# Kernel tuning notes

Hardware: AMD Instinct MI355X
Metric: run time of the kernel (lower is better)

Reference implementation:

```python
import jax, jax.numpy as jnp
import numpy as np

N = 50000
E = 400000
F_IN = 128
HID = 64
HEADS = 4
OUT_HEADS = 4
N_CLS = 121
NEG_SLOPE = 0.2


def _gat_layer(x, src, dst, W, a_src, a_dst, b, heads, out_ch, concat):
    n = x.shape[0]
    xh = (x @ W).reshape(n, heads, out_ch)                      # [N,H,C]
    alpha_s = jnp.sum(xh * a_src, axis=-1)                      # [N,H]
    alpha_d = jnp.sum(xh * a_dst, axis=-1)                      # [N,H]
    logits = jax.nn.leaky_relu(alpha_s[src] + alpha_d[dst], NEG_SLOPE)  # [E,H]
    # numerically stable edge softmax per destination node
    m = jax.ops.segment_max(logits, dst, num_segments=n)        # [N,H]
    e = jnp.exp(logits - m[dst])                                # [E,H]
    denom = jax.ops.segment_sum(e, dst, num_segments=n)         # [N,H]
    alpha = e / (denom[dst] + 1e-16)                            # [E,H]
    msg = alpha[:, :, None] * xh[src]                           # [E,H,C]
    out = jax.ops.segment_sum(msg, dst, num_segments=n)         # [N,H,C]
    if concat:
        out = out.reshape(n, heads * out_ch)
    else:
        out = out.mean(axis=1)
    return out + b


def setup_inputs() -> dict:
    key = jax.random.key(0)
    ks = jax.random.split(key, 20)
    x = jax.random.normal(ks[0], (N, F_IN), dtype=jnp.float32)
    edge_index = jax.random.randint(ks[1], (2, E), 0, N, dtype=jnp.int32)
    s = lambda *sh: 1.0 / np.sqrt(sh[0])
    inp = {
        'x': x,
        'edge_index': edge_index,
        # conv1: F_IN -> HEADS*HID
        'W1': jax.random.normal(ks[2], (F_IN, HEADS * HID), jnp.float32) * s(F_IN),
        'a1_src': jax.random.normal(ks[3], (HEADS, HID), jnp.float32) * s(HID),
        'a1_dst': jax.random.normal(ks[4], (HEADS, HID), jnp.float32) * s(HID),
        'b1': jnp.zeros((HEADS * HID,), jnp.float32),
        'lin1_W': jax.random.normal(ks[5], (F_IN, HEADS * HID), jnp.float32) * s(F_IN),
        'lin1_b': jnp.zeros((HEADS * HID,), jnp.float32),
        # conv2: HEADS*HID -> HEADS*HID
        'W2': jax.random.normal(ks[6], (HEADS * HID, HEADS * HID), jnp.float32) * s(HEADS * HID),
        'a2_src': jax.random.normal(ks[7], (HEADS, HID), jnp.float32) * s(HID),
        'a2_dst': jax.random.normal(ks[8], (HEADS, HID), jnp.float32) * s(HID),
        'b2': jnp.zeros((HEADS * HID,), jnp.float32),
        # conv3: HEADS*HID -> N_CLS (mean over OUT_HEADS)
        'W3': jax.random.normal(ks[9], (HEADS * HID, OUT_HEADS * N_CLS), jnp.float32) * s(HEADS * HID),
        'a3_src': jax.random.normal(ks[10], (OUT_HEADS, N_CLS), jnp.float32) * s(N_CLS),
        'a3_dst': jax.random.normal(ks[11], (OUT_HEADS, N_CLS), jnp.float32) * s(N_CLS),
        'b3': jnp.zeros((N_CLS,), jnp.float32),
        'lin3_W': jax.random.normal(ks[12], (HEADS * HID, N_CLS), jnp.float32) * s(HEADS * HID),
        'lin3_b': jnp.zeros((N_CLS,), jnp.float32),
    }
    return inp


def reference(x, edge_index, W1, a1_src, a1_dst, b1, lin1_W, lin1_b,
              W2, a2_src, a2_dst, b2, W3, a3_src, a3_dst, b3, lin3_W, lin3_b):
    src, dst = edge_index[0], edge_index[1]
    h = _gat_layer(x, src, dst, W1, a1_src, a1_dst, b1, HEADS, HID, True) + (x @ lin1_W + lin1_b)
    h = jax.nn.elu(h)
    h = _gat_layer(h, src, dst, W2, a2_src, a2_dst, b2, HEADS, HID, True) + h  # residual skip (no lin2)
    h = jax.nn.elu(h)
    out = _gat_layer(h, src, dst, W3, a3_src, a3_dst, b3, OUT_HEADS, N_CLS, False) + (h @ lin3_W + lin3_b)
    return out
```

## Files before the change

kernel.cpp:

```cpp
#include <hip/hip_runtime.h>
#include <cstdint>
#include <cstddef>

#define F_IN 128
#define HC12 256
#define HC3P 512
#define NCLS 121
#define L3STR 128

typedef unsigned short u16;
typedef unsigned int u32;
typedef __attribute__((ext_vector_type(8))) short short8;
typedef __attribute__((ext_vector_type(8))) __fp16 half8;
typedef __attribute__((ext_vector_type(4))) float float4v;

static __device__ __forceinline__ float lrelu(float x) { return x > 0.f ? x : 0.2f * x; }

static __device__ __forceinline__ u16 f2h(float f) {
    union { __fp16 h; u16 u; } v; v.h = (__fp16)f; return v.u;
}
static __device__ __forceinline__ float h2f(u16 u) {
    union { u16 u; __fp16 h; } v; v.u = u; return (float)v.h;
}

static __device__ __forceinline__ void gload16(const u16* g, u16* l) {
    __builtin_amdgcn_global_load_lds((const __attribute__((address_space(1))) void*)g,
                                     (__attribute__((address_space(3))) void*)l,
                                     16, 0, 0);
}

__global__ void hist_kernel(const int* __restrict__ dst, int* __restrict__ deg, int E) {
    int e = blockIdx.x * 256 + threadIdx.x;
    if (e < E) atomicAdd(&deg[dst[e]], 1);
}

__global__ __launch_bounds__(1024) void scan_kernel(const int* __restrict__ deg,
                                                    int* __restrict__ rowp, int N) {
    __shared__ int swave[16];
    __shared__ int s_carry;
    int tid = threadIdx.x;
    int w = tid >> 6, lane = tid & 63;
    if (tid == 0) { rowp[0] = 0; s_carry = 0; }
    __syncthreads();
    for (int base = 0; base < N; base += 4096) {
        int i0 = base + tid * 4;
        int v0 = (i0     < N) ? deg[i0]     : 0;
        int v1 = (i0 + 1 < N) ? deg[i0 + 1] : 0;
        int v2 = (i0 + 2 < N) ? deg[i0 + 2] : 0;
        int v3 = (i0 + 3 < N) ? deg[i0 + 3] : 0;
        int t = v0 + v1 + v2 + v3;
        int sc = t;
#pragma unroll
        for (int off = 1; off < 64; off <<= 1) {
            int u = __shfl_up(sc, off, 64);
            if (lane >= off) sc += u;
        }
        if (lane == 63) swave[w] = sc;
        __syncthreads();
        if (w == 0) {
            int ws = (lane < 16) ? swave[lane] : 0;
#pragma unroll
            for (int off = 1; off < 16; off <<= 1) {
                int u = __shfl_up(ws, off, 64);
                if (lane >= off) ws += u;
            }
            if (lane < 16) swave[lane] = ws;
        }
        __syncthreads();
        int carry = s_carry;
        int tb = carry + ((w > 0) ? swave[w - 1] : 0) + sc - t;
        if (i0     < N) rowp[i0 + 1] = tb + v0;
        if (i0 + 1 < N) rowp[i0 + 2] = tb + v0 + v1;
        if (i0 + 2 < N) rowp[i0 + 3] = tb + v0 + v1 + v2;
        if (i0 + 3 < N) rowp[i0 + 4] = tb + t;
        __syncthreads();
        if (tid == 1023) s_carry = carry + swave[15];
        __syncthreads();
    }
}

__global__ void scatter_kernel(const int* __restrict__ src, const int* __restrict__ dst,
                               const int* __restrict__ rowp, int* __restrict__ cur,
                               int* __restrict__ col, int E) {
    int e = blockIdx.x * 256 + threadIdx.x;
    if (e < E) {
        int d = dst[e];
        int pos = rowp[d] + atomicAdd(&cur[d], 1);
        col[pos] = src[e];
    }
}

__global__ void cvtT_all_kernel(const float* W1, const float* l1W, const float* W2,
                                const float* W3, const float* l3W,
                                const float* a3s, const float* a3d,
                                u16* C1, u16* C2, u16* C3,
                                float* as3p, float* ad3p) {
    int i = blockIdx.x * 256 + threadIdx.x;
    if (i >= 285952) {
        int j = i - 285952;
        if (j < 1024) {
            int t = j >> 9, k = j & 511;
            int h = k >> 7, c = k & 127;
            const float* a = t ? a3d : a3s;
            float v = (c < NCLS) ? a[h * NCLS + c] : 0.f;
            (t ? ad3p : as3p)[k] = v;
        }
        return;
    }
    const float* B; u16* o; int K, N;
    if (i < 32768)       { B = W1;  o = C1;             K = 128; N = 256; }
    else if (i < 65536)  { B = l1W; o = C1 + 256 * 128; K = 128; N = 256; i -= 32768; }
    else if (i < 131072) { B = W2;  o = C2;             K = 256; N = 256; i -= 65536; }
    else if (i < 254976) { B = W3;  o = C3;             K = 256; N = 484; i -= 131072; }
    else                 { B = l3W; o = C3 + 484 * 256; K = 256; N = 121; i -= 254976; }
    int n = i % N, k = i / N;
    o[(size_t)n * K + k] = f2h(B[(size_t)k * N + n]);
}

__global__ __launch_bounds__(256) void xcvt_kernel(const float* __restrict__ x,
                                                   u16* __restrict__ o, int total8) {
    int i = blockIdx.x * 256 + threadIdx.x;
    if (i >= total8) return;
    const float4* p = (const float4*)(x + (size_t)i * 8);
    float4 a = p[0], b = p[1];
    union { u16 u[8]; short8 v; } r;
    r.u[0] = f2h(a.x); r.u[1] = f2h(a.y); r.u[2] = f2h(a.z); r.u[3] = f2h(a.w);
    r.u[4] = f2h(b.x); r.u[5] = f2h(b.y); r.u[6] = f2h(b.z); r.u[7] = f2h(b.w);
    *(short8*)(o + (size_t)i * 8) = r.v;
}

#define BM 128
#define BN 128
#define BK 32

__global__ __launch_bounds__(256, 3) void gemm_f16(const u16* __restrict__ A16,
                                                   const u16* __restrict__ BT,
                                                   int M, int K, int Ntot,
                                                   int nx, int ny,
                                                   int Nb, u16* __restrict__ Cb, int strideB,
                                                   int pad121,
                                                   u16* __restrict__ Cf16,
                                                   const float* __restrict__ biasf, int strideF) {
    __shared__ __align__(16) u16 sA[BM * BK];
    __shared__ __align__(16) u16 sB[BN * BK];
    int tid = threadIdx.x;
    int wave = tid >> 6, lane = tid & 63;
    int wr = wave >> 1, wc = wave & 1;

    int bid = blockIdx.x;
    int G = nx * 8;
    int g = bid / G;
    int rem = ny - g * 8;
    int rb, cb;
    if (rem >= 8) {
        int r = bid - g * G;
        rb = g * 8 + (r & 7);
        cb = r >> 3;
    } else {
        int t = bid - g * G;
        rb = g * 8 + t % rem;
        cb = t / rem;
    }
    int m0 = rb * BM, n0 = cb * BN;

    int fm = lane & 15;
    int q = lane >> 4;

    int srow = lane >> 2;
    int sch = (lane & 3) * 8;
    u16* lA0 = &sA[(wave * 32) * BK];
    u16* lA1 = &sA[(wave * 32 + 16) * BK];
    u16* lB0 = &sB[(wave * 32) * BK];
    u16* lB1 = &sB[(wave * 32 + 16) * BK];
    int ar0 = min(m0 + wave * 32 + srow, M - 1);
    int ar1 = min(m0 + wave * 32 + 16 + srow, M - 1);
    int br0 = min(n0 + wave * 32 + srow, Ntot - 1);
    int br1 = min(n0 + wave * 32 + 16 + srow, Ntot - 1);

    float4v acc[4][4];
#pragma unroll
    for (int i = 0; i < 4; i++)
#pragma unroll
        for (int j = 0; j < 4; j++) acc[i][j] = (float4v){0.f, 0.f, 0.f, 0.f};

    for (int kc = 0; kc < K; kc += BK) {
        gload16(&A16[(size_t)ar0 * K + kc + sch], lA0);
        gload16(&A16[(size_t)ar1 * K + kc + sch], lA1);
        gload16(&BT[(size_t)br0 * K + kc + sch], lB0);
        gload16(&BT[(size_t)br1 * K + kc + sch], lB1);
        __syncthreads();

        half8 ah[4];
#pragma unroll
        for (int mi = 0; mi < 4; mi++)
            ah[mi] = *(const half8*)&sA[(wr * 64 + mi * 16 + fm) * BK + q * 8];
#pragma unroll
        for (int ni = 0; ni < 4; ni++) {
            half8 bh = *(const half8*)&sB[(wc * 64 + ni * 16 + fm) * BK + q * 8];
#pragma unroll
            for (int mi = 0; mi < 4; mi++)
                acc[mi][ni] = __builtin_amdgcn_mfma_f32_16x16x32_f16(ah[mi], bh, acc[mi][ni], 0, 0, 0);
        }
        __syncthreads();
    }

#pragma unroll
    for (int mi = 0; mi < 4; mi++) {
#pragma unroll
        for (int ni = 0; ni < 4; ni++) {
            int colg = n0 + wc * 64 + ni * 16 + fm;
            if (colg >= Ntot) continue;
            int cg = colg;
            if (pad121 && colg < Nb) {
                int hh = (colg * 1084) >> 17;
                cg = colg + 7 * hh;
            }
#pragma unroll
            for (int r = 0; r < 4; r++) {
                int rowg = m0 + wr * 64 + mi * 16 + q * 4 + r;
                if (rowg >= M) continue;
                float v = acc[mi][ni][r];
                if (colg < Nb) {
                    Cb[(size_t)rowg * strideB + cg] = f2h(v);
                } else {
                    int cf = colg - Nb;
                    Cf16[(size_t)rowg * strideF + cf] = f2h(v + biasf[cf]);
                }
            }
        }
    }
}

__global__ __launch_bounds__(256) void alpha_wave_256(const u16* __restrict__ xh,
                                                      const float* __restrict__ a_s,
                                                      const float* __restrict__ a_d,
                                                      float* __restrict__ as_o,
                                                      float* __restrict__ ad_o, int N) {
    int lane = threadIdx.x & 63;
    int n = blockIdx.x * 4 + (threadIdx.x >> 6);
    if (n >= N) return;
    int c = lane * 4;
    uint2 v = *(const uint2*)&xh[(size_t)n * HC12 + c];
    float4 s4 = *(const float4*)&a_s[c];
    float4 d4 = *(const float4*)&a_d[c];
    float x0 = h2f((u16)(v.x & 0xffff)), x1 = h2f((u16)(v.x >> 16));
    float x2 = h2f((u16)(v.y & 0xffff)), x3 = h2f((u16)(v.y >> 16));
    float ss = x0 * s4.x + x1 * s4.y + x2 * s4.z + x3 * s4.w;
    float sd = x0 * d4.x + x1 * d4.y + x2 * d4.z + x3 * d4.w;
#pragma unroll
    for (int o = 1; o < 16; o <<= 1) {
        ss += __shfl_xor(ss, o, 64);
        sd += __shfl_xor(sd, o, 64);
    }
    if ((lane & 15) == 0) {
        as_o[n * 4 + (lane >> 4)] = ss;
        ad_o[n * 4 + (lane >> 4)] = sd;
    }
}

__global__ __launch_bounds__(256) void alpha3_wave(const u16* __restrict__ xh3,
                                                   const float* __restrict__ as3p,
                                                   const float* __restrict__ ad3p,
                                                   float* __restrict__ as_o,
                                                   float* __restrict__ ad_o, int N) {
    int l = threadIdx.x & 63;
    int n = blockIdx.x * 4 + (threadIdx.x >> 6);
    if (n >= N) return;
    int h = l >> 4, li = l & 15;
    int c0 = li * 8;
    uint4 v = *(const uint4*)&xh3[(size_t)n * HC3P + l * 8];
    float4 s0 = *(const float4*)&as3p[l * 8];
    float4 s1 = *(const float4*)&as3p[l * 8 + 4];
    float4 d0 = *(const float4*)&ad3p[l * 8];
    float4 d1 = *(const float4*)&ad3p[l * 8 + 4];
    u32 ww[4] = {v.x, v.y, v.z, v.w};
    float xs[8];
#pragma unroll
    for (int j = 0; j < 8; j++) {
        float xf = h2f((u16)((ww[j >> 1] >> ((j & 1) * 16)) & 0xffff));
        xs[j] = (c0 + j < NCLS) ? xf : 0.f;
    }
    float ss = xs[0] * s0.x + xs[1] * s0.y + xs[2] * s0.z + xs[3] * s0.w
             + xs[4] * s1.x + xs[5] * s1.y + xs[6] * s1.z + xs[7] * s1.w;
    float sd = xs[0] * d0.x + xs[1] * d0.y + xs[2] * d0.z + xs[3] * d0.w
             + xs[4] * d1.x + xs[5] * d1.y + xs[6] * d1.z + xs[7] * d1.w;
#pragma unroll
    for (int o = 1; o < 16; o <<= 1) {
        ss += __shfl_xor(ss, o, 64);
        sd += __shfl_xor(sd, o, 64);
    }
    if (li == 0) {
        as_o[n * 4 + h] = ss;
        ad_o[n * 4 + h] = sd;
    }
}

__global__ __launch_bounds__(256) void stats_wave(const int* __restrict__ rowp,
                                                  const int* __restrict__ col,
                                                  const float* __restrict__ asrc,
                                                  const float* __restrict__ adst,
                                                  float* __restrict__ alphaE, int N) {
    int l = threadIdx.x & 63;
    int n = blockIdx.x * 4 + (threadIdx.x >> 6);
    if (n >= N) return;
    int r0 = rowp[n], r1 = rowp[n + 1];
    if (r0 == r1) return;
    int h = l & 3, el = l >> 2;
    float ad = adst[n * 4 + h];
    if (r1 - r0 <= 16) {
        int e = r0 + el;
        bool v = e < r1;
        int sc = col[v ? e : r0];
        float lg = lrelu(asrc[sc * 4 + h] + ad);
        float m = v ? lg : -3.4e38f;
#pragma unroll
        for (int o = 4; o < 64; o <<= 1) m = fmaxf(m, __shfl_xor(m, o, 64));
        float ex = v ? __expf(lg - m) : 0.f;
        float s = ex;
#pragma unroll
        for (int o = 4; o < 64; o <<= 1) s += __shfl_xor(s, o, 64);
        if (v) alphaE[(size_t)e * 4 + h] = ex / (s + 1e-16f);
    } else {
        float m = -3.4e38f, s = 0.f;
        for (int kb = r0; kb < r1; kb += 16) {
            int e = kb + el;
            bool v = e < r1;
            int sc = col[v ? e : r0];
            float lg = lrelu(asrc[sc * 4 + h] + ad);
            float cm = v ? lg : -3.4e38f;
#pragma unroll
            for (int o = 4; o < 64; o <<= 1) cm = fmaxf(cm, __shfl_xor(cm, o, 64));
            float nm = fmaxf(m, cm);
            float ex = v ? __expf(lg - nm) : 0.f;
            float cs = ex;
#pragma unroll
            for (int o = 4; o < 64; o <<= 1) cs += __shfl_xor(cs, o, 64);
            s = s * __expf(m - nm) + cs;
            m = nm;
        }
        float rd = 1.f / (s + 1e-16f);
        for (int kb = r0; kb < r1; kb += 16) {
            int e = kb + el;
            if (e < r1) {
                int sc = col[e];
                float lg = lrelu(asrc[sc * 4 + h] + ad);
                alphaE[(size_t)e * 4 + h] = __expf(lg - m) * rd;
            }
        }
    }
}

__global__ __launch_bounds__(256) void agg_wave_256(const u16* __restrict__ xh,
                                                    const int* __restrict__ rowp,
                                                    const int* __restrict__ col,
                                                    const float* __restrict__ alphaE,
                                                    const float* __restrict__ bias,
                                                    const u16* __restrict__ res16,
                                                    u16* __restrict__ out16, int N) {
    int l = threadIdx.x & 63;
    int n = blockIdx.x * 4 + (threadIdx.x >> 6);
    if (n >= N) return;
    int r0 = rowp[n], r1 = rowp[n + 1];
    int s = l >> 5, li = l & 31;
    int c = li * 8;
    int h = li >> 3;
    float acc[8] = {0.f, 0.f, 0.f, 0.f, 0.f, 0.f, 0.f, 0.f};
    for (int kb = r0; kb < r1; kb += 16) {
        int cn = min(16, r1 - kb);
        int cidx = col[kb + (l & 15)];
        float alv = alphaE[(size_t)kb * 4 + l];
        int npair = (cn + 1) >> 1;
#pragma unroll 4
        for (int k = 0; k < npair; k++) {
            int e = 2 * k + s;
            int em = e < cn ? e : cn - 1;
            int src = __shfl(cidx, em, 64);
            float al = __shfl(alv, em * 4 + h, 64);
            if (e >= cn) al = 0.f;
            uint4 v = *(const uint4*)&xh[(size_t)src * HC12 + c];
            acc[0] += al * h2f((u16)(v.x & 0xffff));
            acc[1] += al * h2f((u16)(v.x >> 16));
            acc[2] += al * h2f((u16)(v.y & 0xffff));
            acc[3] += al * h2f((u16)(v.y >> 16));
            acc[4] += al * h2f((u16)(v.z & 0xffff));
            acc[5] += al * h2f((u16)(v.z >> 16));
            acc[6] += al * h2f((u16)(v.w & 0xffff));
            acc[7] += al * h2f((u16)(v.w >> 16));
        }
    }
#pragma unroll
    for (int j = 0; j < 8; j++) acc[j] += __shfl_xor(acc[j], 32, 64);
    if (l < 32) {
        uint4 rv = *(const uint4*)&res16[(size_t)n * HC12 + c];
        u32 rw[4] = {rv.x, rv.y, rv.z, rv.w};
        float4 b0 = *(const float4*)&bias[c];
        float4 b1v = *(const float4*)&bias[c + 4];
        float bb[8] = {b0.x, b0.y, b0.z, b0.w, b1v.x, b1v.y, b1v.z, b1v.w};
        union { u16 u[8]; uint4 v; } p;
#pragma unroll
        for (int j = 0; j < 8; j++) {
            float rf = h2f((u16)((rw[j >> 1] >> ((j & 1) * 16)) & 0xffff));
            float vv = acc[j] + bb[j] + rf;
            float ev = vv > 0.f ? vv : expm1f(vv);
            p.u[j] = f2h(ev);
        }
        *(uint4*)&out16[(size_t)n * HC12 + c] = p.v;
    }
}

__global__ __launch_bounds__(256) void agg_wave_out(const u16* __restrict__ xh3,
                                                    const int* __restrict__ rowp,
                                                    const int* __restrict__ col,
                                                    const float* __restrict__ alphaE,
                                                    const float* __restrict__ b3,
                                                    const u16* __restrict__ lin3h,
                                                    float* __restrict__ out, int N) {
    int l = threadIdx.x & 63;
    int half = l >> 5, li = l & 31;
    int bl = l & 32;
    int n = blockIdx.x * 8 + (threadIdx.x >> 6) * 2 + half;
    bool nv = n < N;
    int r0 = nv ? rowp[n] : 0;
    int r1 = nv ? rowp[n + 1] : 0;
    float acc[16];
#pragma unroll
    for (int j = 0; j < 16; j++) acc[j] = 0.f;
    for (int kb = r0; kb < r1; kb += 8) {
        int ec = min(8, r1 - kb);
        int ce = kb + (li & 7);
        int cidx = col[ce < r1 ? ce : r0];
        float alv = alphaE[(size_t)kb * 4 + li];
        for (int k = 0; k < ec; k++) {
            int src = __shfl(cidx, bl + k, 64);
            float al = __shfl(alv, bl + k * 4 + (li >> 3), 64);
            const u16* row = xh3 + (size_t)src * HC3P + li * 16;
            uint4 v0 = *(const uint4*)&row[0];
            uint4 v1 = *(const uint4*)&row[8];
            u32 w0[4] = {v0.x, v0.y, v0.z, v0.w};
            u32 w1[4] = {v1.x, v1.y, v1.z, v1.w};
#pragma unroll
            for (int jj = 0; jj < 4; jj++) {
                acc[2 * jj]     += al * h2f((u16)(w0[jj] & 0xffff));
                acc[2 * jj + 1] += al * h2f((u16)(w0[jj] >> 16));
                acc[8 + 2 * jj]     += al * h2f((u16)(w1[jj] & 0xffff));
                acc[8 + 2 * jj + 1] += al * h2f((u16)(w1[jj] >> 16));
            }
        }
    }
#pragma unroll
    for (int j = 0; j < 16; j++) {
        acc[j] += __shfl_xor(acc[j], 8, 64);
        acc[j] += __shfl_xor(acc[j], 16, 64);
    }
    if (nv && li < 8) {
        int c0 = li * 16;
        uint4 l0 = *(const uint4*)&lin3h[(size_t)n * L3STR + c0];
        uint4 l1 = *(const uint4*)&lin3h[(size_t)n * L3STR + c0 + 8];
        u32 lw[8] = {l0.x, l0.y, l0.z, l0.w, l1.x, l1.y, l1.z, l1.w};
#pragma unroll
        for (int j = 0; j < 16; j++) {
            int cc = c0 + j;
            if (cc < NCLS) {
                float lf = h2f((u16)((lw[j >> 1] >> ((j & 1) * 16)) & 0xffff));
                out[(size_t)n * NCLS + cc] = 0.25f * acc[j] + b3[cc] + lf;
            }
        }
    }
}

extern "C" void kernel_launch(void* const* d_in, const int* in_sizes, int n_in,
                              void* d_out, int out_size, void* d_ws, size_t ws_size,
                              hipStream_t stream) {
    const float* x   = (const float*)d_in[0];
    const int*   ei  = (const int*)d_in[1];
    const float* W1  = (const float*)d_in[2];
    const float* a1s = (const float*)d_in[3];
    const float* a1d = (const float*)d_in[4];
    const float* b1  = (const float*)d_in[5];
    const float* l1W = (const float*)d_in[6];
    const float* l1b = (const float*)d_in[7];
    const float* W2  = (const float*)d_in[8];
    const float* a2s = (const float*)d_in[9];
    const float* a2d = (const float*)d_in[10];
    const float* b2  = (const float*)d_in[11];
    const float* W3  = (const float*)d_in[12];
    const float* a3s = (const float*)d_in[13];
    const float* a3d = (const float*)d_in[14];
    const float* b3  = (const float*)d_in[15];
    const float* l3W = (const float*)d_in[16];
    const float* l3b = (const float*)d_in[17];

    const int N = in_sizes[0] / F_IN;
    const int E = in_sizes[1] / 2;
    const int* srcv = ei;
    const int* dstv = ei + E;

    char* ws = (char*)d_ws;
    size_t off = 0;
    auto alloc = [&](size_t bytes) -> char* {
        char* p = ws + off;
        off += (bytes + 255) & ~(size_t)255;
        return p;
    };
    u16*   xh    = (u16*)alloc((size_t)N * HC3P * 2 + 256);
    u16*   x16   = (u16*)alloc((size_t)N * F_IN * 2);
    u16*   h1f   = (u16*)alloc((size_t)N * HC12 * 2);
    u16*   h2f   = (u16*)alloc((size_t)N * HC12 * 2);
    u16*   lin1h = (u16*)alloc((size_t)N * HC12 * 2);
    u16*   lin3h = (u16*)alloc((size_t)N * L3STR * 2);
    float* as_   = (float*)alloc((size_t)N * 4 * 4);
    float* ad_   = (float*)alloc((size_t)N * 4 * 4);
    int* rowp    = (int*)alloc((size_t)(N + 1) * 4);
    int* degc    = (int*)alloc((size_t)N * 4);
    int* cur     = (int*)alloc((size_t)N * 4);
    int* col     = (int*)alloc((size_t)E * 4 + 256);
    float* alphaE = (float*)alloc((size_t)E * 4 * 4 + 256);
    u16* C1 = (u16*)alloc((size_t)512 * 128 * 2);
    u16* C2 = (u16*)alloc((size_t)256 * 256 * 2);
    u16* C3 = (u16*)alloc((size_t)605 * 256 * 2);
    float* as3p = (float*)alloc(512 * 4);
    float* ad3p = (float*)alloc(512 * 4);
    (void)ws_size; (void)n_in; (void)out_size;

    hipMemsetAsync(degc, 0, (size_t)N * 4, stream);
    hipMemsetAsync(cur, 0, (size_t)N * 4, stream);
    hist_kernel<<<(E + 255) / 256, 256, 0, stream>>>(dstv, degc, E);
    scan_kernel<<<1, 1024, 0, stream>>>(degc, rowp, N);
    scatter_kernel<<<(E + 255) / 256, 256, 0, stream>>>(srcv, dstv, rowp, cur, col, E);

    cvtT_all_kernel<<<(285952 + 1024 + 255) / 256, 256, 0, stream>>>(W1, l1W, W2, W3, l3W,
                                                                     a3s, a3d, C1, C2, C3,
                                                                     as3p, ad3p);
    xcvt_kernel<<<(N * F_IN / 8 + 255) / 256, 256, 0, stream>>>(x, x16, N * F_IN / 8);

    int ny = (N + BM - 1) / BM;
    int wgrid = (N + 3) / 4;
    int wgrid8 = (N + 7) / 8;

    gemm_f16<<<4 * ny, 256, 0, stream>>>(x16, C1, N, F_IN, 512, 4, ny,
                                         256, xh, 256, 0, lin1h, l1b, 256);
    alpha_wave_256<<<wgrid, 256, 0, stream>>>(xh, a1s, a1d, as_, ad_, N);
    stats_wave<<<wgrid, 256, 0, stream>>>(rowp, col, as_, ad_, alphaE, N);
    agg_wave_256<<<wgrid, 256, 0, stream>>>(xh, rowp, col, alphaE, b1, lin1h, h1f, N);

    gemm_f16<<<2 * ny, 256, 0, stream>>>(h1f, C2, N, HC12, 256, 2, ny,
                                         256, xh, 256, 0, nullptr, nullptr, 0);
    alpha_wave_256<<<wgrid, 256, 0, stream>>>(xh, a2s, a2d, as_, ad_, N);
    stats_wave<<<wgrid, 256, 0, stream>>>(rowp, col, as_, ad_, alphaE, N);
    agg_wave_256<<<wgrid, 256, 0, stream>>>(xh, rowp, col, alphaE, b2, h1f, h2f, N);

    gemm_f16<<<5 * ny, 256, 0, stream>>>(h2f, C3, N, HC12, 605, 5, ny,
                                         484, xh, HC3P, 1, lin3h, l3b, L3STR);
    alpha3_wave<<<wgrid, 256, 0, stream>>>(xh, as3p, ad3p, as_, ad_, N);
    stats_wave<<<wgrid, 256, 0, stream>>>(rowp, col, as_, ad_, alphaE, N);
    agg_wave_out<<<wgrid8, 256, 0, stream>>>(xh, rowp, col, alphaE, b3, lin3h, (float*)d_out, N);
}
```

Baseline: 500.0 us.

## Fuse edge softmax into aggregation with online rescaling; parallelize degree scan

Removes the separate stats kernel and the per-edge alpha buffer. The aggregation kernels now compute logits, a running max and a running sum per chunk, rescale their accumulators online, and divide by the denominator at the end. This saves three launches and the alphaE write/read traffic, at the cost of extra shuffles and exp work inside the aggregation loop. The single-block scan is also replaced by a three-kernel multi-block scan so building CSR is no longer serialized on one workgroup.

```diff
diff --git a/kernel.cpp b/kernel.cpp
--- a/kernel.cpp
+++ b/kernel.cpp
@@ -34,49 +34,75 @@
     if (e < E) atomicAdd(&deg[dst[e]], 1);
 }
 
-__global__ __launch_bounds__(1024) void scan_kernel(const int* __restrict__ deg,
-                                                    int* __restrict__ rowp, int N) {
-    __shared__ int swave[16];
-    __shared__ int s_carry;
+__global__ __launch_bounds__(256) void scan_part(const int* __restrict__ deg,
+                                                 int* __restrict__ part, int N) {
+    int b = blockIdx.x;
+    int i0 = b * 1024 + threadIdx.x * 4;
+    int t = 0;
+    if (i0     < N) t += deg[i0];
+    if (i0 + 1 < N) t += deg[i0 + 1];
+    if (i0 + 2 < N) t += deg[i0 + 2];
+    if (i0 + 3 < N) t += deg[i0 + 3];
+#pragma unroll
+    for (int o = 1; o < 64; o <<= 1) t += __shfl_xor(t, o, 64);
+    __shared__ int sw[4];
+    int w = threadIdx.x >> 6, lane = threadIdx.x & 63;
+    if (!lane) sw[w] = t;
+    __syncthreads();
+    if (threadIdx.x == 0) part[b] = sw[0] + sw[1] + sw[2] + sw[3];
+}
+
+__global__ void scan_mid(int* __restrict__ part, int nb) {
+    int lane = threadIdx.x;
+    __shared__ int carry_s;
+    if (lane == 0) carry_s = 0;
+    __syncthreads();
+    for (int base = 0; base < nb; base += 64) {
+        int i = base + lane;
+        int v = (i < nb) ? part[i] : 0;
+        int sc = v;
+#pragma unroll
+        for (int o = 1; o < 64; o <<= 1) {
+            int u = __shfl_up(sc, o, 64);
+            if (lane >= o) sc += u;
+        }
+        int carry = carry_s;
+        if (i < nb) part[i] = carry + sc - v;
+        __syncthreads();
+        if (lane == 63) carry_s = carry + sc;
+        __syncthreads();
+    }
+}
+
+__global__ __launch_bounds__(256) void scan_final(const int* __restrict__ deg,
+                                                  const int* __restrict__ part,
+                                                  int* __restrict__ rowp, int N) {
+    int b = blockIdx.x;
     int tid = threadIdx.x;
     int w = tid >> 6, lane = tid & 63;
-    if (tid == 0) { rowp[0] = 0; s_carry = 0; }
+    int i0 = b * 1024 + tid * 4;
+    int v0 = (i0     < N) ? deg[i0]     : 0;
+    int v1 = (i0 + 1 < N) ? deg[i0 + 1] : 0;
+    int v2 = (i0 + 2 < N) ? deg[i0 + 2] : 0;
+    int v3 = (i0 + 3 < N) ? deg[i0 + 3] : 0;
+    int t = v0 + v1 + v2 + v3;
+    int sc = t;
+#pragma unroll
+    for (int o = 1; o < 64; o <<= 1) {
+        int u = __shfl_up(sc, o, 64);
+        if (lane >= o) sc += u;
+    }
+    __shared__ int sw2[4];
+    if (lane == 63) sw2[w] = sc;
     __syncthreads();
-    for (int base = 0; base < N; base += 4096) {
-        int i0 = base + tid * 4;
-        int v0 = (i0     < N) ? deg[i0]     : 0;
-        int v1 = (i0 + 1 < N) ? deg[i0 + 1] : 0;
-        int v2 = (i0 + 2 < N) ? deg[i0 + 2] : 0;
-        int v3 = (i0 + 3 < N) ? deg[i0 + 3] : 0;
-        int t = v0 + v1 + v2 + v3;
-        int sc = t;
-#pragma unroll
-        for (int off = 1; off < 64; off <<= 1) {
-            int u = __shfl_up(sc, off, 64);
-            if (lane >= off) sc += u;
-        }
-        if (lane == 63) swave[w] = sc;
-        __syncthreads();
-        if (w == 0) {
-            int ws = (lane < 16) ? swave[lane] : 0;
-#pragma unroll
-            for (int off = 1; off < 16; off <<= 1) {
-                int u = __shfl_up(ws, off, 64);
-                if (lane >= off) ws += u;
-            }
-            if (lane < 16) swave[lane] = ws;
-        }
-        __syncthreads();
-        int carry = s_carry;
-        int tb = carry + ((w > 0) ? swave[w - 1] : 0) + sc - t;
-        if (i0     < N) rowp[i0 + 1] = tb + v0;
-        if (i0 + 1 < N) rowp[i0 + 2] = tb + v0 + v1;
-        if (i0 + 2 < N) rowp[i0 + 3] = tb + v0 + v1 + v2;
-        if (i0 + 3 < N) rowp[i0 + 4] = tb + t;
-        __syncthreads();
-        if (tid == 1023) s_carry = carry + swave[15];
-        __syncthreads();
-    }
+    int cw = 0;
+    for (int x = 0; x < w; x++) cw += sw2[x];
+    int tb = part[b] + cw + sc - t;
+    if (i0     < N) rowp[i0 + 1] = tb + v0;
+    if (i0 + 1 < N) rowp[i0 + 2] = tb + v0 + v1;
+    if (i0 + 2 < N) rowp[i0 + 3] = tb + v0 + v1 + v2;
+    if (i0 + 3 < N) rowp[i0 + 4] = tb + t;
+    if (b == 0 && tid == 0) rowp[0] = 0;
 }
 
 __global__ void scatter_kernel(const int* __restrict__ src, const int* __restrict__ dst,
@@ -295,87 +321,53 @@
     }
 }
 
-__global__ __launch_bounds__(256) void stats_wave(const int* __restrict__ rowp,
-                                                  const int* __restrict__ col,
-                                                  const float* __restrict__ asrc,
-                                                  const float* __restrict__ adst,
-                                                  float* __restrict__ alphaE, int N) {
+__global__ __launch_bounds__(256) void agg_fused_256(const u16* __restrict__ xh,
+                                                     const int* __restrict__ rowp,
+                                                     const int* __restrict__ col,
+                                                     const float* __restrict__ asrc,
+                                                     const float* __restrict__ adst,
+                                                     const float* __restrict__ bias,
+                                                     const u16* __restrict__ res16,
+                                                     u16* __restrict__ out16, int N) {
     int l = threadIdx.x & 63;
     int n = blockIdx.x * 4 + (threadIdx.x >> 6);
     if (n >= N) return;
     int r0 = rowp[n], r1 = rowp[n + 1];
-    if (r0 == r1) return;
-    int h = l & 3, el = l >> 2;
-    float ad = adst[n * 4 + h];
-    if (r1 - r0 <= 16) {
-        int e = r0 + el;
-        bool v = e < r1;
-        int sc = col[v ? e : r0];
-        float lg = lrelu(asrc[sc * 4 + h] + ad);
-        float m = v ? lg : -3.4e38f;
-#pragma unroll
-        for (int o = 4; o < 64; o <<= 1) m = fmaxf(m, __shfl_xor(m, o, 64));
-        float ex = v ? __expf(lg - m) : 0.f;
-        float s = ex;
-#pragma unroll
-        for (int o = 4; o < 64; o <<= 1) s += __shfl_xor(s, o, 64);
-        if (v) alphaE[(size_t)e * 4 + h] = ex / (s + 1e-16f);
-    } else {
-        float m = -3.4e38f, s = 0.f;
-        for (int kb = r0; kb < r1; kb += 16) {
-            int e = kb + el;
-            bool v = e < r1;
-            int sc = col[v ? e : r0];
-            float lg = lrelu(asrc[sc * 4 + h] + ad);
-            float cm = v ? lg : -3.4e38f;
-#pragma unroll
-            for (int o = 4; o < 64; o <<= 1) cm = fmaxf(cm, __shfl_xor(cm, o, 64));
-            float nm = fmaxf(m, cm);
-            float ex = v ? __expf(lg - nm) : 0.f;
-            float cs = ex;
-#pragma unroll
-            for (int o = 4; o < 64; o <<= 1) cs += __shfl_xor(cs, o, 64);
-            s = s * __expf(m - nm) + cs;
-            m = nm;
-        }
-        float rd = 1.f / (s + 1e-16f);
-        for (int kb = r0; kb < r1; kb += 16) {
-            int e = kb + el;
-            if (e < r1) {
-                int sc = col[e];
-                float lg = lrelu(asrc[sc * 4 + h] + ad);
-                alphaE[(size_t)e * 4 + h] = __expf(lg - m) * rd;
-            }
-        }
-    }
-}
-
-__global__ __launch_bounds__(256) void agg_wave_256(const u16* __restrict__ xh,
-                                                    const int* __restrict__ rowp,
-                                                    const int* __restrict__ col,
-                                                    const float* __restrict__ alphaE,
-                                                    const float* __restrict__ bias,
-                                                    const u16* __restrict__ res16,
-                                                    u16* __restrict__ out16, int N) {
-    int l = threadIdx.x & 63;
-    int n = blockIdx.x * 4 + (threadIdx.x >> 6);
-    if (n >= N) return;
-    int r0 = rowp[n], r1 = rowp[n + 1];
-    int s = l >> 5, li = l & 31;
+    int s_slot = l >> 5, li = l & 31;
     int c = li * 8;
     int h = li >> 3;
+    int hs = l & 3;
+    int e_st = l >> 2;
+    float ad = adst[n * 4 + hs];
+    float m = -3.4e38f, ssum = 0.f;
     float acc[8] = {0.f, 0.f, 0.f, 0.f, 0.f, 0.f, 0.f, 0.f};
     for (int kb = r0; kb < r1; kb += 16) {
         int cn = min(16, r1 - kb);
         int cidx = col[kb + (l & 15)];
-        float alv = alphaE[(size_t)kb * 4 + l];
+        int esc = __shfl(cidx, e_st, 64);
+        bool ev = e_st < cn;
+        float lg = ev ? lrelu(asrc[esc * 4 + hs] + ad) : -3.4e38f;
+        float cm = lg;
+#pragma unroll
+        for (int o = 4; o < 64; o <<= 1) cm = fmaxf(cm, __shfl_xor(cm, o, 64));
+        float mn = fmaxf(m, cm);
+        float es = __expf(m - mn);
+        float atil = ev ? __expf(lg - mn) : 0.f;
+        float cs = atil;
+#pragma unroll
+        for (int o = 4; o < 64; o <<= 1) cs += __shfl_xor(cs, o, 64);
+        ssum = ssum * es + cs;
+        m = mn;
+        float eso = __shfl(es, (l & 60) | h, 64);
+#pragma unroll
+        for (int j = 0; j < 8; j++) acc[j] *= eso;
         int npair = (cn + 1) >> 1;
 #pragma unroll 4
         for (int k = 0; k < npair; k++) {
-            int e = 2 * k + s;
+            int e = 2 * k + s_slot;
             int em = e < cn ? e : cn - 1;
             int src = __shfl(cidx, em, 64);
-            float al = __shfl(alv, em * 4 + h, 64);
+            float al = __shfl(atil, em * 4 + h, 64);
             if (e >= cn) al = 0.f;
             uint4 v = *(const uint4*)&xh[(size_t)src * HC12 + c];
             acc[0] += al * h2f((u16)(v.x & 0xffff));
@@ -388,6 +380,8 @@
             acc[7] += al * h2f((u16)(v.w >> 16));
         }
     }
+    float sso = __shfl(ssum, (l & 60) | h, 64);
+    float inv = 1.f / (sso + 1e-16f);
 #pragma unroll
     for (int j = 0; j < 8; j++) acc[j] += __shfl_xor(acc[j], 32, 64);
     if (l < 32) {
@@ -400,21 +394,22 @@
 #pragma unroll
         for (int j = 0; j < 8; j++) {
             float rf = h2f((u16)((rw[j >> 1] >> ((j & 1) * 16)) & 0xffff));
-            float vv = acc[j] + bb[j] + rf;
-            float ev = vv > 0.f ? vv : expm1f(vv);
-            p.u[j] = f2h(ev);
+            float vv = acc[j] * inv + bb[j] + rf;
+            float ev2 = vv > 0.f ? vv : expm1f(vv);
+            p.u[j] = f2h(ev2);
         }
         *(uint4*)&out16[(size_t)n * HC12 + c] = p.v;
     }
 }
 
-__global__ __launch_bounds__(256) void agg_wave_out(const u16* __restrict__ xh3,
-                                                    const int* __restrict__ rowp,
-                                                    const int* __restrict__ col,
-                                                    const float* __restrict__ alphaE,
-                                                    const float* __restrict__ b3,
-                                                    const u16* __restrict__ lin3h,
-                                                    float* __restrict__ out, int N) {
+__global__ __launch_bounds__(256) void agg_fused_out(const u16* __restrict__ xh3,
+                                                     const int* __restrict__ rowp,
+                                                     const int* __restrict__ col,
+                                                     const float* __restrict__ asrc,
+                                                     const float* __restrict__ adst,
+                                                     const float* __restrict__ b3,
+                                                     const u16* __restrict__ lin3h,
+                                                     float* __restrict__ out, int N) {
     int l = threadIdx.x & 63;
     int half = l >> 5, li = l & 31;
     int bl = l & 32;
@@ -422,17 +417,38 @@
     bool nv = n < N;
     int r0 = nv ? rowp[n] : 0;
     int r1 = nv ? rowp[n + 1] : 0;
+    int h = li >> 3;
+    int hs = li & 3;
+    int e_st = li >> 2;
+    float ad = nv ? adst[n * 4 + hs] : 0.f;
+    float m = -3.4e38f, ssum = 0.f;
     float acc[16];
 #pragma unroll
     for (int j = 0; j < 16; j++) acc[j] = 0.f;
     for (int kb = r0; kb < r1; kb += 8) {
-        int ec = min(8, r1 - kb);
+        int cn = min(8, r1 - kb);
         int ce = kb + (li & 7);
         int cidx = col[ce < r1 ? ce : r0];
-        float alv = alphaE[(size_t)kb * 4 + li];
-        for (int k = 0; k < ec; k++) {
+        int esc = __shfl(cidx, bl + e_st, 64);
+        bool ev = e_st < cn;
+        float lg = ev ? lrelu(asrc[esc * 4 + hs] + ad) : -3.4e38f;
+        float cm = lg;
+#pragma unroll
+        for (int o = 4; o < 32; o <<= 1) cm = fmaxf(cm, __shfl_xor(cm, o, 64));
+        float mn = fmaxf(m, cm);
+        float es = __expf(m - mn);
+        float atil = ev ? __expf(lg - mn) : 0.f;
+        float cs = atil;
+#pragma unroll
+        for (int o = 4; o < 32; o <<= 1) cs += __shfl_xor(cs, o, 64);
+        ssum = ssum * es + cs;
+        m = mn;
+        float eso = __shfl(es, bl + ((li & 28) | h), 64);
+#pragma unroll
+        for (int j = 0; j < 16; j++) acc[j] *= eso;
+        for (int k = 0; k < cn; k++) {
             int src = __shfl(cidx, bl + k, 64);
-            float al = __shfl(alv, bl + k * 4 + (li >> 3), 64);
+            float al = __shfl(atil, bl + k * 4 + h, 64);
             const u16* row = xh3 + (size_t)src * HC3P + li * 16;
             uint4 v0 = *(const uint4*)&row[0];
             uint4 v1 = *(const uint4*)&row[8];
@@ -447,6 +463,10 @@
             }
         }
     }
+    float sso = __shfl(ssum, bl + ((li & 28) | h), 64);
+    float inv = 1.f / (sso + 1e-16f);
+#pragma unroll
+    for (int j = 0; j < 16; j++) acc[j] *= inv;
 #pragma unroll
     for (int j = 0; j < 16; j++) {
         acc[j] += __shfl_xor(acc[j], 8, 64);
@@ -513,8 +533,8 @@
     int* rowp    = (int*)alloc((size_t)(N + 1) * 4);
     int* degc    = (int*)alloc((size_t)N * 4);
     int* cur     = (int*)alloc((size_t)N * 4);
+    int* part    = (int*)alloc((size_t)256 * 4);
     int* col     = (int*)alloc((size_t)E * 4 + 256);
-    float* alphaE = (float*)alloc((size_t)E * 4 * 4 + 256);
     u16* C1 = (u16*)alloc((size_t)512 * 128 * 2);
     u16* C2 = (u16*)alloc((size_t)256 * 256 * 2);
     u16* C3 = (u16*)alloc((size_t)605 * 256 * 2);
@@ -525,7 +545,10 @@
     hipMemsetAsync(degc, 0, (size_t)N * 4, stream);
     hipMemsetAsync(cur, 0, (size_t)N * 4, stream);
     hist_kernel<<<(E + 255) / 256, 256, 0, stream>>>(dstv, degc, E);
-    scan_kernel<<<1, 1024, 0, stream>>>(degc, rowp, N);
+    int nb = (N + 1023) / 1024;
+    scan_part<<<nb, 256, 0, stream>>>(degc, part, N);
+    scan_mid<<<1, 64, 0, stream>>>(part, nb);
+    scan_final<<<nb, 256, 0, stream>>>(degc, part, rowp, N);
     scatter_kernel<<<(E + 255) / 256, 256, 0, stream>>>(srcv, dstv, rowp, cur, col, E);
 
     cvtT_all_kernel<<<(285952 + 1024 + 255) / 256, 256, 0, stream>>>(W1, l1W, W2, W3, l3W,
@@ -540,18 +563,16 @@
     gemm_f16<<<4 * ny, 256, 0, stream>>>(x16, C1, N, F_IN, 512, 4, ny,
                                          256, xh, 256, 0, lin1h, l1b, 256);
     alpha_wave_256<<<wgrid, 256, 0, stream>>>(xh, a1s, a1d, as_, ad_, N);
-    stats_wave<<<wgrid, 256, 0, stream>>>(rowp, col, as_, ad_, alphaE, N);
-    agg_wave_256<<<wgrid, 256, 0, stream>>>(xh, rowp, col, alphaE, b1, lin1h, h1f, N);
+    agg_fused_256<<<wgrid, 256, 0, stream>>>(xh, rowp, col, as_, ad_, b1, lin1h, h1f, N);
 
     gemm_f16<<<2 * ny, 256, 0, stream>>>(h1f, C2, N, HC12, 256, 2, ny,
                                          256, xh, 256, 0, nullptr, nullptr, 0);
     alpha_wave_256<<<wgrid, 256, 0, stream>>>(xh, a2s, a2d, as_, ad_, N);
-    stats_wave<<<wgrid, 256, 0, stream>>>(rowp, col, as_, ad_, alphaE, N);
-    agg_wave_256<<<wgrid, 256, 0, stream>>>(xh, rowp, col, alphaE, b2, h1f, h2f, N);
+    agg_fused_256<<<wgrid, 256, 0, stream>>>(xh, rowp, col, as_, ad_, b2, h1f, h2f, N);
 
     gemm_f16<<<5 * ny, 256, 0, stream>>>(h2f, C3, N, HC12, 605, 5, ny,
                                          484, xh, HC3P, 1, lin3h, l3b, L3STR);
     alpha3_wave<<<wgrid, 256, 0, stream>>>(xh, as3p, ad3p, as_, ad_, N);
-    stats_wave<<<wgrid, 256, 0, stream>>>(rowp, col, as_, ad_, alphaE, N);
-    agg_wave_out<<<wgrid8, 256, 0, stream>>>(xh, rowp, col, alphaE, b3, lin3h, (float*)d_out, N);
-}
+    agg_fused_out<<<wgrid8, 256, 0, stream>>>(xh, rowp, col, as_, ad_, b3, lin3h,
+                                              (float*)d_out, N);
+}
```

Measured after the change: 449.0 us. 10.2% less time.
